# Kernel tuning notes

Measured on AMD Instinct MI355X. Metric: run time of the kernel, lower is better.

## Reference

```python
import jax, jax.numpy as jnp
import numpy as np

N_NODES = 50000
N_EDGES = 800000
IN_DIM = 128
OUT_DIM = 128
NUM_RELS = 8


def setup_inputs() -> dict:
    key = jax.random.key(0)
    k_feat, k_rel, k_w, k_src, k_dst, k_rt = jax.random.split(key, 6)
    feat = jax.random.normal(k_feat, (N_NODES, IN_DIM), dtype=jnp.float32)
    # xavier_uniform over (in_dim, out_dim) fan
    limit = float(np.sqrt(6.0 / (IN_DIM + OUT_DIM)))
    rel_emb = jax.random.uniform(k_rel, (NUM_RELS, IN_DIM, OUT_DIM), dtype=jnp.float32,
                                 minval=-limit, maxval=limit)
    edge_weight = jax.random.uniform(k_w, (N_EDGES,), dtype=jnp.float32)
    src = jax.random.randint(k_src, (N_EDGES,), 0, N_NODES, dtype=jnp.int32)
    dst = jax.random.randint(k_dst, (N_EDGES,), 0, N_NODES, dtype=jnp.int32)
    rel_type = jax.random.randint(k_rt, (N_EDGES,), 0, NUM_RELS, dtype=jnp.int32)
    return {"feat": feat, "rel_emb": rel_emb, "edge_weight": edge_weight,
            "src": src, "dst": dst, "rel_type": rel_type}


def reference(feat, rel_emb, edge_weight, src, dst, rel_type):
    # src_feat: [E, in] gather of source-node features
    src_feat = feat[src]
    num_rels = rel_emb.shape[0]
    # Equivalent to bmm(src_feat[:,None,:], rel_emb[rel_type]).squeeze(1)
    # but avoids materializing the [E, in, out] per-edge weight tensor:
    # loop over the small fixed relation set with masked accumulation.
    msg = jnp.zeros((src_feat.shape[0], rel_emb.shape[2]), dtype=src_feat.dtype)
    for r in range(num_rels):
        mask = (rel_type == r)[:, None]
        msg = msg + jnp.where(mask, src_feat @ rel_emb[r], jnp.zeros((), dtype=src_feat.dtype))
    msg = msg * edge_weight[:, None]
    # copy_e + sum aggregation onto destination nodes: [N, out]
    return jax.ops.segment_sum(msg, dst, num_segments=feat.shape[0])
```

## Files before the change

kernel.cpp:

```cpp
#include <hip/hip_runtime.h>
#include <stdint.h>

#define N_NODES   50000
#define N_EDGES   800000
#define IN_DIM    128
#define OUT_DIM   128
#define NUM_RELS  8
#define THREADS   256

typedef _Float16 half_t;
typedef _Float16 half2v __attribute__((ext_vector_type(2)));
typedef _Float16 half4v __attribute__((ext_vector_type(4)));
typedef _Float16 half8 __attribute__((ext_vector_type(8)));
typedef float floatx4 __attribute__((ext_vector_type(4)));


#define NBINS3    N_NODES
#define NB3       ((NBINS3 + 1023) / 1024)

#define WS_Y2     0
#define WS_OFF    102400000
#define WS_WT     102600064
#define WS_BASE   102862208
#define WS_WGT    106062208
#define WS_HIST   107662208
#define WS_BSUM   107862208
#define WS_NEED   (size_t)107862464

__global__ void prep_hist_kernel(const float* __restrict__ rel_emb, half_t* __restrict__ WT,
                                 const int* __restrict__ dst, int* __restrict__ hist) {
    int b = blockIdx.x;
    if (b < 512) {
        int t = b * 256 + threadIdx.x;
        int r = t >> 14, k = (t >> 7) & 127, n = t & 127;
        WT[(size_t)((r << 7) | n) * 128 + k] = (half_t)rel_emb[t];
    } else {
        int i = (b - 512) * 256 + threadIdx.x;
        if (i < N_EDGES) atomicAdd(&hist[dst[i]], 1);
    }
}

__global__ void scan1_kernel(const int* __restrict__ hist, int* __restrict__ bsum) {
    __shared__ int sh[256];
    int b = blockIdx.x, t = threadIdx.x;
    int i0 = b * 1024 + t * 4;
    int s = 0;
    #pragma unroll
    for (int j = 0; j < 4; j++) { int idx = i0 + j; if (idx < NBINS3) s += hist[idx]; }
    sh[t] = s; __syncthreads();
    for (int o = 128; o > 0; o >>= 1) { if (t < o) sh[t] += sh[t + o]; __syncthreads(); }
    if (t == 0) bsum[b] = sh[0];
}

__global__ void scan2_kernel(int* __restrict__ bsum, int* __restrict__ off) {
    __shared__ int sh[64];
    int t = threadIdx.x;
    int v = (t < NB3) ? bsum[t] : 0;
    sh[t] = v; __syncthreads();
    for (int o = 1; o < 64; o <<= 1) {
        int x = (t >= o) ? sh[t - o] : 0;
        __syncthreads();
        sh[t] += x;
        __syncthreads();
    }
    if (t < NB3) bsum[t] = sh[t] - v;
    if (t == 0) off[NBINS3] = N_EDGES;
}

__global__ void scan3_kernel(const int* __restrict__ hist, const int* __restrict__ boff,
                             int* __restrict__ off, int* __restrict__ cursors) {
    __shared__ int sh[256];
    int b = blockIdx.x, t = threadIdx.x;
    int i0 = b * 1024 + t * 4;
    int v[4]; int s = 0;
    #pragma unroll
    for (int j = 0; j < 4; j++) { int idx = i0 + j; v[j] = (idx < NBINS3) ? hist[idx] : 0; s += v[j]; }
    sh[t] = s; __syncthreads();
    for (int o = 1; o < 256; o <<= 1) {
        int x = (t >= o) ? sh[t - o] : 0;
        __syncthreads();
        sh[t] += x;
        __syncthreads();
    }
    int run = sh[t] - s + boff[b];
    #pragma unroll
    for (int j = 0; j < 4; j++) {
        int idx = i0 + j;
        if (idx < NBINS3) { off[idx] = run; cursors[idx] = run; }
        run += v[j];
    }
}

__global__ void scatter3_kernel(const int* __restrict__ dst, const int* __restrict__ src,
                                const int* __restrict__ rel, const float* __restrict__ ew,
                                int* __restrict__ cursors, int* __restrict__ base,
                                half_t* __restrict__ wgt) {
    int i = blockIdx.x * blockDim.x + threadIdx.x;
    if (i < N_EDGES) {
        int pos = atomicAdd(&cursors[dst[i]], 1);
        base[pos] = src[i] * 1024 + rel[i] * 128;
        wgt[pos] = (half_t)ew[i];
    }
}

template<bool GUARD>
__device__ __forceinline__ void gemm_body(const float* __restrict__ feat,
                                          const half_t* __restrict__ Ws,
                                          half_t* __restrict__ y2,
                                          int m0, int n0, int wave, int lane) {
    const int q = lane >> 4, l16 = lane & 15;
    const int wm0 = m0 + wave * 32;

    float4 fr[2][4][2];
    #pragma unroll
    for (int ms = 0; ms < 2; ms++) {
        int node = wm0 + ms * 16 + l16;
        const float* fb = feat + (size_t)node * 128 + q * 8;
        bool ok = !GUARD || node < N_NODES;
        #pragma unroll
        for (int kk = 0; kk < 4; kk++)
            #pragma unroll
            for (int h = 0; h < 2; h++) {
                float4 v = {0.f, 0.f, 0.f, 0.f};
                if (ok) v = *(const float4*)(fb + kk * 32 + h * 4);
                fr[ms][kk][h] = v;
            }
    }
    __syncthreads();

    half8 bf[2][4];
    #pragma unroll
    for (int ms = 0; ms < 2; ms++)
        #pragma unroll
        for (int kk = 0; kk < 4; kk++) {
            half8 hb;
            hb[0] = (half_t)fr[ms][kk][0].x; hb[1] = (half_t)fr[ms][kk][0].y;
            hb[2] = (half_t)fr[ms][kk][0].z; hb[3] = (half_t)fr[ms][kk][0].w;
            hb[4] = (half_t)fr[ms][kk][1].x; hb[5] = (half_t)fr[ms][kk][1].y;
            hb[6] = (half_t)fr[ms][kk][1].z; hb[7] = (half_t)fr[ms][kk][1].w;
            bf[ms][kk] = hb;
        }

    floatx4 acc[8][2];
    #pragma unroll
    for (int nt = 0; nt < 8; nt++)
        #pragma unroll
        for (int ms = 0; ms < 2; ms++) acc[nt][ms] = (floatx4){0.f, 0.f, 0.f, 0.f};

    #pragma unroll
    for (int kk = 0; kk < 4; kk++) {
        #pragma unroll
        for (int nt = 0; nt < 8; nt++) {
            int row = nt * 16 + l16;
            int phys = (kk * 4 + q) ^ (l16 & 7);
            half8 a = *(const half8*)(Ws + row * 128 + phys * 8);
            acc[nt][0] = __builtin_amdgcn_mfma_f32_16x16x32_f16(a, bf[0][kk], acc[nt][0], 0, 0, 0);
            acc[nt][1] = __builtin_amdgcn_mfma_f32_16x16x32_f16(a, bf[1][kk], acc[nt][1], 0, 0, 0);
        }
    }

    #pragma unroll
    for (int nt = 0; nt < 8; nt++)
        #pragma unroll
        for (int ms = 0; ms < 2; ms++) {
            int node = wm0 + ms * 16 + l16;
            int nn = n0 + nt * 16 + q * 4;
            if (!GUARD || node < N_NODES) {
                half4v hv;
                hv[0] = (half_t)acc[nt][ms][0]; hv[1] = (half_t)acc[nt][ms][1];
                hv[2] = (half_t)acc[nt][ms][2]; hv[3] = (half_t)acc[nt][ms][3];
                *(half4v*)(y2 + (size_t)node * 1024 + nn) = hv;
            }
        }
}

#define GY_GRID (391 * 8)
__global__ __launch_bounds__(THREADS) void gemm_y_kernel(
    const float* __restrict__ feat, const half_t* __restrict__ WT,
    half_t* __restrict__ y2) {
    __shared__ half_t Ws[128 * 128];
    int bid = blockIdx.x;
    int work = (bid & 7) * 391 + (bid >> 3);
    int mt = work >> 3, nt8 = work & 7;
    const int m0 = mt * 128, n0 = nt8 * 128;
    const int t = threadIdx.x;
    const int wave = t >> 6, lane = t & 63;

    for (int i = t; i < 2048; i += THREADS) {
        int row = i >> 4, lc = i & 15;
        int phys = lc ^ (row & 7);
        *(uint4*)&Ws[row * 128 + phys * 8] =
            *(const uint4*)(WT + (size_t)(n0 + row) * 128 + lc * 8);
    }
    if (m0 + 128 <= N_NODES)
        gemm_body<false>(feat, Ws, y2, m0, n0, wave, lane);
    else
        gemm_body<true>(feat, Ws, y2, m0, n0, wave, lane);
}

__global__ __launch_bounds__(THREADS) void gather_kernel(
    const half_t* __restrict__ y2, const int* __restrict__ base,
    const half_t* __restrict__ wgt, const int* __restrict__ off,
    float* __restrict__ out) {
    int g = blockIdx.x * 4 + (threadIdx.x >> 6);
    int lane = threadIdx.x & 63;
    int beg = off[g], end = off[g + 1];
    const half_t* yb = y2 + lane * 2;
    float ax = 0.f, ay = 0.f, cx = 0.f, cy = 0.f;
    int e = beg;
    for (; e + 8 <= end; e += 8) {
        int b0 = base[e], b1 = base[e + 1], b2 = base[e + 2], b3 = base[e + 3];
        int b4 = base[e + 4], b5 = base[e + 5], b6 = base[e + 6], b7 = base[e + 7];
        half2v v0 = *(const half2v*)(yb + b0);
        half2v v1 = *(const half2v*)(yb + b1);
        half2v v2 = *(const half2v*)(yb + b2);
        half2v v3 = *(const half2v*)(yb + b3);
        half2v v4 = *(const half2v*)(yb + b4);
        half2v v5 = *(const half2v*)(yb + b5);
        half2v v6 = *(const half2v*)(yb + b6);
        half2v v7 = *(const half2v*)(yb + b7);
        float w0 = (float)wgt[e],     w1 = (float)wgt[e + 1];
        float w2 = (float)wgt[e + 2], w3 = (float)wgt[e + 3];
        float w4 = (float)wgt[e + 4], w5 = (float)wgt[e + 5];
        float w6 = (float)wgt[e + 6], w7 = (float)wgt[e + 7];
        ax += w0 * (float)v0[0] + w1 * (float)v1[0];
        ay += w0 * (float)v0[1] + w1 * (float)v1[1];
        cx += w2 * (float)v2[0] + w3 * (float)v3[0];
        cy += w2 * (float)v2[1] + w3 * (float)v3[1];
        ax += w4 * (float)v4[0] + w5 * (float)v5[0];
        ay += w4 * (float)v4[1] + w5 * (float)v5[1];
        cx += w6 * (float)v6[0] + w7 * (float)v7[0];
        cy += w6 * (float)v6[1] + w7 * (float)v7[1];
    }
    for (; e + 2 <= end; e += 2) {
        int b0 = base[e], b1 = base[e + 1];
        float w0 = (float)wgt[e], w1 = (float)wgt[e + 1];
        half2v v0 = *(const half2v*)(yb + b0);
        half2v v1 = *(const half2v*)(yb + b1);
        ax += w0 * (float)v0[0] + w1 * (float)v1[0];
        ay += w0 * (float)v0[1] + w1 * (float)v1[1];
    }
    if (e < end) {
        int b0 = base[e];
        float w0 = (float)wgt[e];
        half2v v0 = *(const half2v*)(yb + b0);
        cx += w0 * (float)v0[0];
        cy += w0 * (float)v0[1];
    }
    float2 o; o.x = ax + cx; o.y = ay + cy;
    *(float2*)(out + (size_t)g * 128 + lane * 2) = o;
}

__global__ void naive_kernel(const float* __restrict__ feat, const float* __restrict__ rel_emb,
                             const float* __restrict__ ew, const int* __restrict__ src,
                             const int* __restrict__ dst, const int* __restrict__ rel,
                             float* __restrict__ out) {
    int wave = (blockIdx.x * blockDim.x + threadIdx.x) >> 6;
    int lane = threadIdx.x & 63;
    if (wave >= N_EDGES) return;
    const float* f = feat + (size_t)src[wave] * IN_DIM;
    const float* W = rel_emb + (size_t)rel[wave] * IN_DIM * OUT_DIM;
    float w = ew[wave];
    float a0 = 0.f, a1 = 0.f;
    for (int k = 0; k < IN_DIM; k++) {
        float fv = f[k];
        a0 += fv * W[k * OUT_DIM + lane];
        a1 += fv * W[k * OUT_DIM + 64 + lane];
    }
    int d = dst[wave];
    atomicAdd(&out[(size_t)d * OUT_DIM + lane], a0 * w);
    atomicAdd(&out[(size_t)d * OUT_DIM + 64 + lane], a1 * w);
}

extern "C" void kernel_launch(void* const* d_in, const int* in_sizes, int n_in,
                              void* d_out, int out_size, void* d_ws, size_t ws_size,
                              hipStream_t stream) {
    const float* feat    = (const float*)d_in[0];
    const float* rel_emb = (const float*)d_in[1];
    const float* ew      = (const float*)d_in[2];
    const int*   src     = (const int*)d_in[3];
    const int*   dst     = (const int*)d_in[4];
    const int*   rel     = (const int*)d_in[5];
    float* out = (float*)d_out;

    const int eb = (N_EDGES + THREADS - 1) / THREADS;

    if (ws_size >= WS_NEED) {
        char* ws = (char*)d_ws;
        half_t* y2    = (half_t*)(ws + WS_Y2);
        int*    off   = (int*)(ws + WS_OFF);
        half_t* WT    = (half_t*)(ws + WS_WT);
        int*    basep = (int*)(ws + WS_BASE);
        half_t* wgt   = (half_t*)(ws + WS_WGT);
        int*    hist  = (int*)(ws + WS_HIST);
        int*    bsum  = (int*)(ws + WS_BSUM);

        hipMemsetAsync(hist, 0, (size_t)NBINS3 * 4, stream);
        prep_hist_kernel<<<512 + eb, THREADS, 0, stream>>>(rel_emb, WT, dst, hist);
        gemm_y_kernel<<<GY_GRID, THREADS, 0, stream>>>(feat, WT, y2);
        scan1_kernel<<<NB3, 256, 0, stream>>>(hist, bsum);
        scan2_kernel<<<1, 64, 0, stream>>>(bsum, off);
        scan3_kernel<<<NB3, 256, 0, stream>>>(hist, bsum, off, hist);
        scatter3_kernel<<<eb, THREADS, 0, stream>>>(dst, src, rel, ew, hist, basep, wgt);
        gather_kernel<<<N_NODES / 4, THREADS, 0, stream>>>(y2, basep, wgt, off, out);
    } else {
        hipMemsetAsync(d_out, 0, (size_t)out_size * sizeof(float), stream);
        const long long total = (long long)N_EDGES * 64;
        const int blocks = (int)((total + THREADS - 1) / THREADS);
        naive_kernel<<<blocks, THREADS, 0, stream>>>(feat, rel_emb, ew, src, dst, rel, out);
    }
}
```

Measured before the change: 269.3 us.

## Persist GEMM blocks over four M-tiles, merge scans, widen gather loads

Result: slower. 317.9 us (+18.1%).

```diff
diff --git a/kernel.cpp b/kernel.cpp
--- a/kernel.cpp
+++ b/kernel.cpp
@@ -16,7 +16,6 @@
 
 
 #define NBINS3    N_NODES
-#define NB3       ((NBINS3 + 1023) / 1024)
 
 #define WS_Y2     0
 #define WS_OFF    102400000
@@ -24,7 +23,6 @@
 #define WS_BASE   102862208
 #define WS_WGT    106062208
 #define WS_HIST   107662208
-#define WS_BSUM   107862208
 #define WS_NEED   (size_t)107862464
 
 __global__ void prep_hist_kernel(const float* __restrict__ rel_emb, half_t* __restrict__ WT,
@@ -40,55 +38,35 @@
     }
 }
 
-__global__ void scan1_kernel(const int* __restrict__ hist, int* __restrict__ bsum) {
-    __shared__ int sh[256];
-    int b = blockIdx.x, t = threadIdx.x;
-    int i0 = b * 1024 + t * 4;
-    int s = 0;
-    #pragma unroll
-    for (int j = 0; j < 4; j++) { int idx = i0 + j; if (idx < NBINS3) s += hist[idx]; }
-    sh[t] = s; __syncthreads();
-    for (int o = 128; o > 0; o >>= 1) { if (t < o) sh[t] += sh[t + o]; __syncthreads(); }
-    if (t == 0) bsum[b] = sh[0];
-}
-
-__global__ void scan2_kernel(int* __restrict__ bsum, int* __restrict__ off) {
-    __shared__ int sh[64];
-    int t = threadIdx.x;
-    int v = (t < NB3) ? bsum[t] : 0;
-    sh[t] = v; __syncthreads();
-    for (int o = 1; o < 64; o <<= 1) {
-        int x = (t >= o) ? sh[t - o] : 0;
+__global__ __launch_bounds__(1024) void scan_all_kernel(const int* __restrict__ hist,
+                                                        int* __restrict__ off,
+                                                        int* __restrict__ cursors) {
+    __shared__ int sh[1024];
+    const int t = threadIdx.x;
+    int carry = 0;
+    for (int c = 0; c < 13; c++) {
+        int i0 = c * 4096 + t * 4;
+        int v0 = (i0     < NBINS3) ? hist[i0]     : 0;
+        int v1 = (i0 + 1 < NBINS3) ? hist[i0 + 1] : 0;
+        int v2 = (i0 + 2 < NBINS3) ? hist[i0 + 2] : 0;
+        int v3 = (i0 + 3 < NBINS3) ? hist[i0 + 3] : 0;
+        int s = v0 + v1 + v2 + v3;
+        sh[t] = s; __syncthreads();
+        for (int o = 1; o < 1024; o <<= 1) {
+            int x = (t >= o) ? sh[t - o] : 0;
+            __syncthreads();
+            sh[t] += x;
+            __syncthreads();
+        }
+        int run = carry + sh[t] - s;
+        if (i0     < NBINS3) { off[i0]     = run; cursors[i0]     = run; } run += v0;
+        if (i0 + 1 < NBINS3) { off[i0 + 1] = run; cursors[i0 + 1] = run; } run += v1;
+        if (i0 + 2 < NBINS3) { off[i0 + 2] = run; cursors[i0 + 2] = run; } run += v2;
+        if (i0 + 3 < NBINS3) { off[i0 + 3] = run; cursors[i0 + 3] = run; }
+        carry += sh[1023];
         __syncthreads();
-        sh[t] += x;
-        __syncthreads();
-    }
-    if (t < NB3) bsum[t] = sh[t] - v;
+    }
     if (t == 0) off[NBINS3] = N_EDGES;
-}
-
-__global__ void scan3_kernel(const int* __restrict__ hist, const int* __restrict__ boff,
-                             int* __restrict__ off, int* __restrict__ cursors) {
-    __shared__ int sh[256];
-    int b = blockIdx.x, t = threadIdx.x;
-    int i0 = b * 1024 + t * 4;
-    int v[4]; int s = 0;
-    #pragma unroll
-    for (int j = 0; j < 4; j++) { int idx = i0 + j; v[j] = (idx < NBINS3) ? hist[idx] : 0; s += v[j]; }
-    sh[t] = s; __syncthreads();
-    for (int o = 1; o < 256; o <<= 1) {
-        int x = (t >= o) ? sh[t - o] : 0;
-        __syncthreads();
-        sh[t] += x;
-        __syncthreads();
-    }
-    int run = sh[t] - s + boff[b];
-    #pragma unroll
-    for (int j = 0; j < 4; j++) {
-        int idx = i0 + j;
-        if (idx < NBINS3) { off[idx] = run; cursors[idx] = run; }
-        run += v[j];
-    }
 }
 
 __global__ void scatter3_kernel(const int* __restrict__ dst, const int* __restrict__ src,
@@ -104,14 +82,8 @@
 }
 
 template<bool GUARD>
-__device__ __forceinline__ void gemm_body(const float* __restrict__ feat,
-                                          const half_t* __restrict__ Ws,
-                                          half_t* __restrict__ y2,
-                                          int m0, int n0, int wave, int lane) {
-    const int q = lane >> 4, l16 = lane & 15;
-    const int wm0 = m0 + wave * 32;
-
-    float4 fr[2][4][2];
+__device__ __forceinline__ void load_feat(const float* __restrict__ feat, int wm0,
+                                          int q, int l16, float4 fr[2][4][2]) {
     #pragma unroll
     for (int ms = 0; ms < 2; ms++) {
         int node = wm0 + ms * 16 + l16;
@@ -120,71 +92,87 @@
         #pragma unroll
         for (int kk = 0; kk < 4; kk++)
             #pragma unroll
-            for (int h = 0; h < 2; h++) {
+            for (int hh = 0; hh < 2; hh++) {
                 float4 v = {0.f, 0.f, 0.f, 0.f};
-                if (ok) v = *(const float4*)(fb + kk * 32 + h * 4);
-                fr[ms][kk][h] = v;
-            }
-    }
-    __syncthreads();
-
-    half8 bf[2][4];
+                if (ok) v = *(const float4*)(fb + kk * 32 + hh * 4);
+                fr[ms][kk][hh] = v;
+            }
+    }
+}
+
+template<bool GUARD>
+__device__ __forceinline__ void gemm_mloop(const float* __restrict__ feat,
+                                           const half_t* __restrict__ Ws,
+                                           half_t* __restrict__ y2,
+                                           int msup, int n0, int wave, int lane,
+                                           float4 fr[2][4][2]) {
+    const int q = lane >> 4, l16 = lane & 15;
     #pragma unroll
-    for (int ms = 0; ms < 2; ms++)
+    for (int mi = 0; mi < 4; mi++) {
+        const int wm0 = msup * 512 + mi * 128 + wave * 32;
+        half8 bf[2][4];
+        #pragma unroll
+        for (int ms = 0; ms < 2; ms++)
+            #pragma unroll
+            for (int kk = 0; kk < 4; kk++) {
+                half8 hb;
+                hb[0] = (half_t)fr[ms][kk][0].x; hb[1] = (half_t)fr[ms][kk][0].y;
+                hb[2] = (half_t)fr[ms][kk][0].z; hb[3] = (half_t)fr[ms][kk][0].w;
+                hb[4] = (half_t)fr[ms][kk][1].x; hb[5] = (half_t)fr[ms][kk][1].y;
+                hb[6] = (half_t)fr[ms][kk][1].z; hb[7] = (half_t)fr[ms][kk][1].w;
+                bf[ms][kk] = hb;
+            }
+        if (mi < 3) load_feat<GUARD>(feat, wm0 + 128, q, l16, fr);
+
+        floatx4 acc[8][2];
+        #pragma unroll
+        for (int nt = 0; nt < 8; nt++) {
+            acc[nt][0] = (floatx4){0.f, 0.f, 0.f, 0.f};
+            acc[nt][1] = (floatx4){0.f, 0.f, 0.f, 0.f};
+        }
         #pragma unroll
         for (int kk = 0; kk < 4; kk++) {
-            half8 hb;
-            hb[0] = (half_t)fr[ms][kk][0].x; hb[1] = (half_t)fr[ms][kk][0].y;
-            hb[2] = (half_t)fr[ms][kk][0].z; hb[3] = (half_t)fr[ms][kk][0].w;
-            hb[4] = (half_t)fr[ms][kk][1].x; hb[5] = (half_t)fr[ms][kk][1].y;
-            hb[6] = (half_t)fr[ms][kk][1].z; hb[7] = (half_t)fr[ms][kk][1].w;
-            bf[ms][kk] = hb;
+            int phys = (kk * 4 + q) ^ (l16 & 7);
+            #pragma unroll
+            for (int nt = 0; nt < 8; nt++) {
+                half8 a = *(const half8*)(Ws + (nt * 16 + l16) * 128 + phys * 8);
+                acc[nt][0] = __builtin_amdgcn_mfma_f32_16x16x32_f16(a, bf[0][kk], acc[nt][0], 0, 0, 0);
+                acc[nt][1] = __builtin_amdgcn_mfma_f32_16x16x32_f16(a, bf[1][kk], acc[nt][1], 0, 0, 0);
+            }
         }
-
-    floatx4 acc[8][2];
-    #pragma unroll
-    for (int nt = 0; nt < 8; nt++)
-        #pragma unroll
-        for (int ms = 0; ms < 2; ms++) acc[nt][ms] = (floatx4){0.f, 0.f, 0.f, 0.f};
-
-    #pragma unroll
-    for (int kk = 0; kk < 4; kk++) {
-        #pragma unroll
-        for (int nt = 0; nt < 8; nt++) {
-            int row = nt * 16 + l16;
-            int phys = (kk * 4 + q) ^ (l16 & 7);
-            half8 a = *(const half8*)(Ws + row * 128 + phys * 8);
-            acc[nt][0] = __builtin_amdgcn_mfma_f32_16x16x32_f16(a, bf[0][kk], acc[nt][0], 0, 0, 0);
-            acc[nt][1] = __builtin_amdgcn_mfma_f32_16x16x32_f16(a, bf[1][kk], acc[nt][1], 0, 0, 0);
-        }
-    }
-
-    #pragma unroll
-    for (int nt = 0; nt < 8; nt++)
-        #pragma unroll
-        for (int ms = 0; ms < 2; ms++) {
-            int node = wm0 + ms * 16 + l16;
-            int nn = n0 + nt * 16 + q * 4;
-            if (!GUARD || node < N_NODES) {
-                half4v hv;
-                hv[0] = (half_t)acc[nt][ms][0]; hv[1] = (half_t)acc[nt][ms][1];
-                hv[2] = (half_t)acc[nt][ms][2]; hv[3] = (half_t)acc[nt][ms][3];
-                *(half4v*)(y2 + (size_t)node * 1024 + nn) = hv;
-            }
-        }
-}
-
-#define GY_GRID (391 * 8)
+        #pragma unroll
+        for (int nt = 0; nt < 8; nt++)
+            #pragma unroll
+            for (int ms = 0; ms < 2; ms++) {
+                int node = wm0 + ms * 16 + l16;
+                int nn = n0 + nt * 16 + q * 4;
+                if (!GUARD || node < N_NODES) {
+                    half4v hv;
+                    hv[0] = (half_t)acc[nt][ms][0]; hv[1] = (half_t)acc[nt][ms][1];
+                    hv[2] = (half_t)acc[nt][ms][2]; hv[3] = (half_t)acc[nt][ms][3];
+                    *(half4v*)(y2 + (size_t)node * 1024 + nn) = hv;
+                }
+            }
+    }
+}
+
+#define GY_BLOCKS 784
 __global__ __launch_bounds__(THREADS) void gemm_y_kernel(
     const float* __restrict__ feat, const half_t* __restrict__ WT,
     half_t* __restrict__ y2) {
     __shared__ half_t Ws[128 * 128];
     int bid = blockIdx.x;
-    int work = (bid & 7) * 391 + (bid >> 3);
-    int mt = work >> 3, nt8 = work & 7;
-    const int m0 = mt * 128, n0 = nt8 * 128;
+    int work = (bid & 7) * 98 + (bid >> 3);
+    int msup = work >> 3, nchunk = work & 7;
+    const int n0 = nchunk * 128;
     const int t = threadIdx.x;
     const int wave = t >> 6, lane = t & 63;
+    const int q = lane >> 4, l16 = lane & 15;
+
+    float4 fr[2][4][2];
+    bool guard = (msup == 97);
+    if (!guard) load_feat<false>(feat, msup * 512 + wave * 32, q, l16, fr);
+    else        load_feat<true>(feat, msup * 512 + wave * 32, q, l16, fr);
 
     for (int i = t; i < 2048; i += THREADS) {
         int row = i >> 4, lc = i & 15;
@@ -192,10 +180,10 @@
         *(uint4*)&Ws[row * 128 + phys * 8] =
             *(const uint4*)(WT + (size_t)(n0 + row) * 128 + lc * 8);
     }
-    if (m0 + 128 <= N_NODES)
-        gemm_body<false>(feat, Ws, y2, m0, n0, wave, lane);
-    else
-        gemm_body<true>(feat, Ws, y2, m0, n0, wave, lane);
+    __syncthreads();
+
+    if (!guard) gemm_mloop<false>(feat, Ws, y2, msup, n0, wave, lane, fr);
+    else        gemm_mloop<true>(feat, Ws, y2, msup, n0, wave, lane, fr);
 }
 
 __global__ __launch_bounds__(THREADS) void gather_kernel(
@@ -204,51 +192,46 @@
     float* __restrict__ out) {
     int g = blockIdx.x * 4 + (threadIdx.x >> 6);
     int lane = threadIdx.x & 63;
+    int h = lane >> 5;
+    int c4 = (lane & 31) * 4;
+    const half_t* yb = y2 + c4;
     int beg = off[g], end = off[g + 1];
-    const half_t* yb = y2 + lane * 2;
-    float ax = 0.f, ay = 0.f, cx = 0.f, cy = 0.f;
+    float a0 = 0.f, a1 = 0.f, a2 = 0.f, a3 = 0.f;
     int e = beg;
     for (; e + 8 <= end; e += 8) {
-        int b0 = base[e], b1 = base[e + 1], b2 = base[e + 2], b3 = base[e + 3];
-        int b4 = base[e + 4], b5 = base[e + 5], b6 = base[e + 6], b7 = base[e + 7];
-        half2v v0 = *(const half2v*)(yb + b0);
-        half2v v1 = *(const half2v*)(yb + b1);
-        half2v v2 = *(const half2v*)(yb + b2);
-        half2v v3 = *(const half2v*)(yb + b3);
-        half2v v4 = *(const half2v*)(yb + b4);
-        half2v v5 = *(const half2v*)(yb + b5);
-        half2v v6 = *(const half2v*)(yb + b6);
-        half2v v7 = *(const half2v*)(yb + b7);
-        float w0 = (float)wgt[e],     w1 = (float)wgt[e + 1];
-        float w2 = (float)wgt[e + 2], w3 = (float)wgt[e + 3];
-        float w4 = (float)wgt[e + 4], w5 = (float)wgt[e + 5];
-        float w6 = (float)wgt[e + 6], w7 = (float)wgt[e + 7];
-        ax += w0 * (float)v0[0] + w1 * (float)v1[0];
-        ay += w0 * (float)v0[1] + w1 * (float)v1[1];
-        cx += w2 * (float)v2[0] + w3 * (float)v3[0];
-        cy += w2 * (float)v2[1] + w3 * (float)v3[1];
-        ax += w4 * (float)v4[0] + w5 * (float)v5[0];
-        ay += w4 * (float)v4[1] + w5 * (float)v5[1];
-        cx += w6 * (float)v6[0] + w7 * (float)v7[0];
-        cy += w6 * (float)v6[1] + w7 * (float)v7[1];
+        int b0 = base[e + h],     b1 = base[e + 2 + h];
+        int b2 = base[e + 4 + h], b3 = base[e + 6 + h];
+        half4v v0 = *(const half4v*)(yb + b0);
+        half4v v1 = *(const half4v*)(yb + b1);
+        half4v v2 = *(const half4v*)(yb + b2);
+        half4v v3 = *(const half4v*)(yb + b3);
+        float w0 = (float)wgt[e + h],     w1 = (float)wgt[e + 2 + h];
+        float w2 = (float)wgt[e + 4 + h], w3 = (float)wgt[e + 6 + h];
+        a0 += w0 * (float)v0[0] + w1 * (float)v1[0] + w2 * (float)v2[0] + w3 * (float)v3[0];
+        a1 += w0 * (float)v0[1] + w1 * (float)v1[1] + w2 * (float)v2[1] + w3 * (float)v3[1];
+        a2 += w0 * (float)v0[2] + w1 * (float)v1[2] + w2 * (float)v2[2] + w3 * (float)v3[2];
+        a3 += w0 * (float)v0[3] + w1 * (float)v1[3] + w2 * (float)v2[3] + w3 * (float)v3[3];
     }
     for (; e + 2 <= end; e += 2) {
-        int b0 = base[e], b1 = base[e + 1];
-        float w0 = (float)wgt[e], w1 = (float)wgt[e + 1];
-        half2v v0 = *(const half2v*)(yb + b0);
-        half2v v1 = *(const half2v*)(yb + b1);
-        ax += w0 * (float)v0[0] + w1 * (float)v1[0];
-        ay += w0 * (float)v0[1] + w1 * (float)v1[1];
-    }
-    if (e < end) {
-        int b0 = base[e];
-        float w0 = (float)wgt[e];
-        half2v v0 = *(const half2v*)(yb + b0);
-        cx += w0 * (float)v0[0];
-        cy += w0 * (float)v0[1];
-    }
-    float2 o; o.x = ax + cx; o.y = ay + cy;
-    *(float2*)(out + (size_t)g * 128 + lane * 2) = o;
+        int b = base[e + h];
+        float w = (float)wgt[e + h];
+        half4v v = *(const half4v*)(yb + b);
+        a0 += w * (float)v[0]; a1 += w * (float)v[1];
+        a2 += w * (float)v[2]; a3 += w * (float)v[3];
+    }
+    if (e < end && h == 0) {
+        int b = base[e];
+        float w = (float)wgt[e];
+        half4v v = *(const half4v*)(yb + b);
+        a0 += w * (float)v[0]; a1 += w * (float)v[1];
+        a2 += w * (float)v[2]; a3 += w * (float)v[3];
+    }
+    a0 += __shfl_xor(a0, 32); a1 += __shfl_xor(a1, 32);
+    a2 += __shfl_xor(a2, 32); a3 += __shfl_xor(a3, 32);
+    if (h == 0) {
+        float4 o; o.x = a0; o.y = a1; o.z = a2; o.w = a3;
+        *(float4*)(out + (size_t)g * 128 + c4) = o;
+    }
 }
 
 __global__ void naive_kernel(const float* __restrict__ feat, const float* __restrict__ rel_emb,
@@ -293,14 +276,11 @@
         int*    basep = (int*)(ws + WS_BASE);
         half_t* wgt   = (half_t*)(ws + WS_WGT);
         int*    hist  = (int*)(ws + WS_HIST);
-        int*    bsum  = (int*)(ws + WS_BSUM);
 
         hipMemsetAsync(hist, 0, (size_t)NBINS3 * 4, stream);
         prep_hist_kernel<<<512 + eb, THREADS, 0, stream>>>(rel_emb, WT, dst, hist);
-        gemm_y_kernel<<<GY_GRID, THREADS, 0, stream>>>(feat, WT, y2);
-        scan1_kernel<<<NB3, 256, 0, stream>>>(hist, bsum);
-        scan2_kernel<<<1, 64, 0, stream>>>(bsum, off);
-        scan3_kernel<<<NB3, 256, 0, stream>>>(hist, bsum, off, hist);
+        gemm_y_kernel<<<GY_BLOCKS, THREADS, 0, stream>>>(feat, WT, y2);
+        scan_all_kernel<<<1, 1024, 0, stream>>>(hist, off, hist);
         scatter3_kernel<<<eb, THREADS, 0, stream>>>(dst, src, rel, ew, hist, basep, wgt);
         gather_kernel<<<N_NODES / 4, THREADS, 0, stream>>>(y2, basep, wgt, off, out);
     } else {
```
